# Kernel optimization log

Hardware: AMD Instinct MI355X
Metric: run time of the kernel (lower is better)

## Reference

```python
import jax, jax.numpy as jnp
import numpy as np

B, P, E, H = 32, 16, 50000, 128
EPS = 1e-5


def setup_inputs() -> dict:
    key = jax.random.key(0)
    ks = jax.random.split(key, 8)
    return {
        "inputs": jax.random.randint(ks[0], (B, P, E), 0, 2, dtype=jnp.int32),
        "emb": jax.random.normal(ks[1], (E, H), jnp.float32) * 0.02,
        "w1": jax.random.normal(ks[2], (H, H), jnp.float32) / np.sqrt(H),
        "b1": jax.random.normal(ks[3], (H,), jnp.float32) * 0.01,
        "w2": jax.random.normal(ks[4], (H, H), jnp.float32) / np.sqrt(H),
        "b2": jax.random.normal(ks[5], (H,), jnp.float32) * 0.01,
        "ln1_g": jnp.ones((H,), jnp.float32),
        "ln1_b": jnp.zeros((H,), jnp.float32),
        "ln2_g": jnp.ones((H,), jnp.float32),
        "ln2_b": jnp.zeros((H,), jnp.float32),
        "bn1_g": jnp.ones((H,), jnp.float32),
        "bn1_b": jnp.zeros((H,), jnp.float32),
        "bn2_g": jnp.ones((H,), jnp.float32),
        "bn2_b": jnp.zeros((H,), jnp.float32),
    }


def _layer_norm(x, g, b):
    mu = x.mean(-1, keepdims=True)
    var = ((x - mu) ** 2).mean(-1, keepdims=True)
    return g * (x - mu) / jnp.sqrt(var + EPS) + b


def _batch_norm_eval(x, g, b):
    # eval-mode BatchNorm1d with running_mean=0, running_var=1
    return g * x / jnp.sqrt(1.0 + EPS) + b


def reference(inputs, emb, w1, b1, w2, b2, ln1_g, ln1_b, ln2_g, ln2_b,
              bn1_g, bn1_b, bn2_g, bn2_b):
    # padding_idx=0: embedding row 0 is zero (but still counted in the mean,
    # matching the torch loop which averages over all selected indices)
    emb0 = emb.at[0].set(0.0)
    mask = (inputs == 1).astype(emb.dtype)            # [B, P, E] multi-hot
    sums = jnp.einsum("bpe,eh->bph", mask, emb0)       # segment-sum as one GEMM
    cnt = mask.sum(-1, keepdims=True)                  # [B, P, 1]
    path_emb = jnp.where(cnt > 0, sums / jnp.maximum(cnt, 1.0), 0.0)
    x = path_emb.mean(axis=1)                          # mean over paths -> [B, H]
    x = _layer_norm(x, ln1_g, ln1_b)
    x = jax.nn.relu(x @ w1.T + b1)
    x = _batch_norm_eval(x, bn1_g, bn1_b)              # dropout = identity (eval)
    x = _layer_norm(x, ln2_g, ln2_b)
    x = jax.nn.relu(x @ w2.T + b2)
    x = _batch_norm_eval(x, bn2_g, bn2_b)
    return x
```

## Files before the change

kernel.cpp:

```cpp
#include <hip/hip_runtime.h>
#include <stdint.h>

#define E_DIM 50000
#define EP    50048
#define HD    128
#define BD    32
#define PD    16
#define MD    512
#define BM    32
#define BK    64
#define KCHUNK 768
#define NKC   66
#define EPSF  1e-5f

typedef short short8 __attribute__((ext_vector_type(8)));
typedef float f32x4  __attribute__((ext_vector_type(4)));

__device__ __forceinline__ uint16_t f2bf(float f) {
  uint32_t u = __float_as_uint(f);
  u += 0x7FFFu + ((u >> 16) & 1u);
  return (uint16_t)(u >> 16);
}

__global__ __launch_bounds__(256) void k_embT(const float* __restrict__ emb,
                                              uint16_t* __restrict__ embT) {
  __shared__ __align__(16) uint16_t lds[HD * 64];
  const int t  = threadIdx.x;
  const int e0 = blockIdx.x * 64;

#pragma unroll
  for (int pass = 0; pass < 8; ++pass) {
    const int el = pass * 8 + (t >> 5);
    const int h  = (t & 31) * 4;
    const int eg = e0 + el;
    float4 v = {0.f, 0.f, 0.f, 0.f};
    if (eg < E_DIM && eg != 0)
      v = *(const float4*)(emb + (size_t)eg * HD + h);
    const uint16_t q0 = f2bf(v.x), q1 = f2bf(v.y), q2 = f2bf(v.z), q3 = f2bf(v.w);
    lds[(h + 0) * 64 + (el ^ (((h + 0) & 7) << 3))] = q0;
    lds[(h + 1) * 64 + (el ^ (((h + 1) & 7) << 3))] = q1;
    lds[(h + 2) * 64 + (el ^ (((h + 2) & 7) << 3))] = q2;
    lds[(h + 3) * 64 + (el ^ (((h + 3) & 7) << 3))] = q3;
  }
  __syncthreads();
#pragma unroll
  for (int pass = 0; pass < 8; ++pass) {
    const int hr  = pass * 16 + (t >> 4);
    const int el4 = (t & 15) * 4;
    uint2 d = *(const uint2*)(lds + hr * 64 + (el4 ^ ((hr & 7) << 3)));
    *(uint2*)(embT + (size_t)hr * EP + e0 + el4) = d;
  }
}

__global__ __launch_bounds__(256, 4) void k_gemm(const int* __restrict__ inp,
                                                 const uint16_t* __restrict__ embT,
                                                 float* __restrict__ part,
                                                 float* __restrict__ cntp) {
  __shared__ __align__(16) uint16_t ldsA[2][BM * BK];
  __shared__ __align__(16) uint16_t ldsB[2][HD * BK];

  const int t    = threadIdx.x;
  const int lane = t & 63;
  const int w    = t >> 6;

  const int virt = (blockIdx.x & 7) * (NKC * 16 / 8) + (blockIdx.x >> 3);
  const int mb = virt & 15;
  const int kc = virt >> 4;
  const int e0 = kc * KCHUNK;
  const int nst = min(12, (EP - e0) >> 6);

  const int sr = t >> 3;
  const int sc = (t & 7) * 8;
  const int* ap = inp + (size_t)(mb * BM + sr) * E_DIM + e0 + sc;
  const int aw = sr * 128 + (((t & 7) ^ (sr & 7)) << 4);

  const int bh = t >> 1;
  const int bq = (t & 1) * 4;
  const uint16_t* bp = embT + (size_t)bh * EP + e0 + bq * 8;
  const int bw0 = bh * 128 + (((bq + 0) ^ (bh & 7)) << 4);
  const int bw1 = bh * 128 + (((bq + 1) ^ (bh & 7)) << 4);
  const int bw2 = bh * 128 + (((bq + 2) ^ (bh & 7)) << 4);
  const int bw3 = bh * 128 + (((bq + 3) ^ (bh & 7)) << 4);

  const int r16 = lane & 15;
  const int kg  = (lane >> 4) << 3;
  const int aoff = r16 * 128;
  const int boff = (w * 32 + r16) * 128;
  const int swr  = r16 & 7;

  f32x4 acc00 = {0.f,0.f,0.f,0.f}, acc01 = {0.f,0.f,0.f,0.f};
  f32x4 acc10 = {0.f,0.f,0.f,0.f}, acc11 = {0.f,0.f,0.f,0.f};
  uint32_t cnt = 0;

  {
    int4 a0 = {0,0,0,0}, a1 = {0,0,0,0};
    if (e0 + sc < E_DIM) { a0 = *(const int4*)ap; a1 = *(const int4*)(ap + 4); }
    const short8 v0 = *(const short8*)(bp);
    const short8 v1 = *(const short8*)(bp + 8);
    const short8 v2 = *(const short8*)(bp + 16);
    const short8 v3 = *(const short8*)(bp + 24);
    const uint32_t w01 = (uint32_t)a0.x | ((uint32_t)a0.y << 16);
    const uint32_t w23 = (uint32_t)a0.z | ((uint32_t)a0.w << 16);
    const uint32_t w45 = (uint32_t)a1.x | ((uint32_t)a1.y << 16);
    const uint32_t w67 = (uint32_t)a1.z | ((uint32_t)a1.w << 16);
    cnt += w01 + w23 + w45 + w67;
    uint4 d = { w01 * 0x3F80u, w23 * 0x3F80u, w45 * 0x3F80u, w67 * 0x3F80u };
    *(uint4*)((char*)ldsA[0] + aw) = d;
    *(short8*)((char*)ldsB[0] + bw0) = v0;
    *(short8*)((char*)ldsB[0] + bw1) = v1;
    *(short8*)((char*)ldsB[0] + bw2) = v2;
    *(short8*)((char*)ldsB[0] + bw3) = v3;
    __syncthreads();
  }

  for (int s = 0; s < nst; ++s) {
    const int cur = s & 1;
    const int nxt = cur ^ 1;
    const bool hn = (s + 1 < nst);
    int4 a0 = {0,0,0,0}, a1 = {0,0,0,0};
    short8 v0, v1, v2, v3;
    if (hn) {
      const int off = (s + 1) * 64;
      if (e0 + off + sc < E_DIM) {
        a0 = *(const int4*)(ap + off);
        a1 = *(const int4*)(ap + off + 4);
      }
      v0 = *(const short8*)(bp + off);
      v1 = *(const short8*)(bp + off + 8);
      v2 = *(const short8*)(bp + off + 16);
      v3 = *(const short8*)(bp + off + 24);
    }

#pragma unroll
    for (int kk = 0; kk < 64; kk += 32) {
      const int cblk = (kk + kg) >> 3;
      const int sw16 = (cblk ^ swr) << 4;
      const short8 af0 = *(const short8*)((const char*)ldsA[cur] + aoff + sw16);
      const short8 af1 = *(const short8*)((const char*)ldsA[cur] + aoff + sw16 + 2048);
      const short8 bf0 = *(const short8*)((const char*)ldsB[cur] + boff + sw16);
      const short8 bf1 = *(const short8*)((const char*)ldsB[cur] + boff + sw16 + 2048);
      acc00 = __builtin_amdgcn_mfma_f32_16x16x32_bf16(af0, bf0, acc00, 0, 0, 0);
      acc01 = __builtin_amdgcn_mfma_f32_16x16x32_bf16(af0, bf1, acc01, 0, 0, 0);
      acc10 = __builtin_amdgcn_mfma_f32_16x16x32_bf16(af1, bf0, acc10, 0, 0, 0);
      acc11 = __builtin_amdgcn_mfma_f32_16x16x32_bf16(af1, bf1, acc11, 0, 0, 0);
    }

    if (hn) {
      const uint32_t w01 = (uint32_t)a0.x | ((uint32_t)a0.y << 16);
      const uint32_t w23 = (uint32_t)a0.z | ((uint32_t)a0.w << 16);
      const uint32_t w45 = (uint32_t)a1.x | ((uint32_t)a1.y << 16);
      const uint32_t w67 = (uint32_t)a1.z | ((uint32_t)a1.w << 16);
      cnt += w01 + w23 + w45 + w67;
      uint4 d = { w01 * 0x3F80u, w23 * 0x3F80u, w45 * 0x3F80u, w67 * 0x3F80u };
      *(uint4*)((char*)ldsA[nxt] + aw) = d;
      *(short8*)((char*)ldsB[nxt] + bw0) = v0;
      *(short8*)((char*)ldsB[nxt] + bw1) = v1;
      *(short8*)((char*)ldsB[nxt] + bw2) = v2;
      *(short8*)((char*)ldsB[nxt] + bw3) = v3;
    }
    __syncthreads();
  }

  {
    const int jr = (lane >> 4) << 2;
    float* pt0 = part + (size_t)kc * (MD * HD)
               + (size_t)(mb * BM + jr) * HD + w * 32 + r16;
#pragma unroll
    for (int j = 0; j < 4; ++j) {
      pt0[j * HD]             = acc00[j];
      pt0[j * HD + 16]        = acc01[j];
      pt0[(16 + j) * HD]      = acc10[j];
      pt0[(16 + j) * HD + 16] = acc11[j];
    }
  }

  {
    int c = (int)((cnt & 0xFFFFu) + (cnt >> 16));
    c += __shfl_xor(c, 1);
    c += __shfl_xor(c, 2);
    c += __shfl_xor(c, 4);
    if ((lane & 7) == 0)
      cntp[kc * MD + mb * BM + w * 8 + (lane >> 3)] = (float)c;
  }
}

__global__ __launch_bounds__(128) void k_reduce(const float* __restrict__ part,
                                                const float* __restrict__ cntp,
                                                float* __restrict__ pe) {
  const int r = blockIdx.x;
  const int t = threadIdx.x;
  const float* pp = part + (size_t)r * HD + t;
  float s = 0.f;
#pragma unroll 6
  for (int kc = 0; kc < NKC; ++kc) s += pp[(size_t)kc * (MD * HD)];
  float c = 0.f;
#pragma unroll 6
  for (int kc = 0; kc < NKC; ++kc) c += cntp[kc * MD + r];
  pe[r * HD + t] = (c > 0.f) ? (s / c) : 0.f;
}

__global__ __launch_bounds__(128) void k_tail(
    const float* __restrict__ pe,
    const float* __restrict__ w1, const float* __restrict__ b1,
    const float* __restrict__ w2, const float* __restrict__ b2,
    const float* __restrict__ ln1g, const float* __restrict__ ln1b,
    const float* __restrict__ ln2g, const float* __restrict__ ln2b,
    const float* __restrict__ bn1g, const float* __restrict__ bn1b,
    const float* __restrict__ bn2g, const float* __restrict__ bn2b,
    float* __restrict__ out) {
  const int b = blockIdx.x, t = threadIdx.x;
  __shared__ float sh[HD];
  __shared__ float red[HD];

  float x = 0.f;
#pragma unroll
  for (int p = 0; p < PD; ++p) x += pe[(b * PD + p) * HD + t];
  x *= (1.f / PD);

  const float bninv = rsqrtf(1.f + EPSF);

  red[t] = x; __syncthreads();
  for (int o = 64; o > 0; o >>= 1) { if (t < o) red[t] += red[t + o]; __syncthreads(); }
  const float mu1 = red[0] * (1.f / HD); __syncthreads();
  const float d1 = x - mu1;
  red[t] = d1 * d1; __syncthreads();
  for (int o = 64; o > 0; o >>= 1) { if (t < o) red[t] += red[t + o]; __syncthreads(); }
  const float v1 = red[0] * (1.f / HD); __syncthreads();
  const float y1 = ln1g[t] * d1 * rsqrtf(v1 + EPSF) + ln1b[t];

  sh[t] = y1; __syncthreads();
  float a = b1[t];
  const float4* wrow1 = (const float4*)(w1 + (size_t)t * HD);
#pragma unroll 8
  for (int k = 0; k < 32; ++k) {
    const float4 w = wrow1[k];
    a += w.x * sh[k * 4] + w.y * sh[k * 4 + 1] + w.z * sh[k * 4 + 2] + w.w * sh[k * 4 + 3];
  }
  a = fmaxf(a, 0.f);
  a = bn1g[t] * a * bninv + bn1b[t];
  __syncthreads();

  red[t] = a; __syncthreads();
  for (int o = 64; o > 0; o >>= 1) { if (t < o) red[t] += red[t + o]; __syncthreads(); }
  const float mu2 = red[0] * (1.f / HD); __syncthreads();
  const float d2 = a - mu2;
  red[t] = d2 * d2; __syncthreads();
  for (int o = 64; o > 0; o >>= 1) { if (t < o) red[t] += red[t + o]; __syncthreads(); }
  const float v2 = red[0] * (1.f / HD); __syncthreads();
  const float y2 = ln2g[t] * d2 * rsqrtf(v2 + EPSF) + ln2b[t];

  sh[t] = y2; __syncthreads();
  float a2 = b2[t];
  const float4* wrow2 = (const float4*)(w2 + (size_t)t * HD);
#pragma unroll 8
  for (int k = 0; k < 32; ++k) {
    const float4 w = wrow2[k];
    a2 += w.x * sh[k * 4] + w.y * sh[k * 4 + 1] + w.z * sh[k * 4 + 2] + w.w * sh[k * 4 + 3];
  }
  a2 = fmaxf(a2, 0.f);
  a2 = bn2g[t] * a2 * bninv + bn2b[t];
  out[b * HD + t] = a2;
}

extern "C" void kernel_launch(void* const* d_in, const int* in_sizes, int n_in,
                              void* d_out, int out_size, void* d_ws, size_t ws_size,
                              hipStream_t stream) {
  const int*   inp  = (const int*)d_in[0];
  const float* emb  = (const float*)d_in[1];
  const float* w1   = (const float*)d_in[2];
  const float* b1   = (const float*)d_in[3];
  const float* w2   = (const float*)d_in[4];
  const float* b2   = (const float*)d_in[5];
  const float* ln1g = (const float*)d_in[6];
  const float* ln1b = (const float*)d_in[7];
  const float* ln2g = (const float*)d_in[8];
  const float* ln2b = (const float*)d_in[9];
  const float* bn1g = (const float*)d_in[10];
  const float* bn1b = (const float*)d_in[11];
  const float* bn2g = (const float*)d_in[12];
  const float* bn2b = (const float*)d_in[13];
  float* out = (float*)d_out;

  char* ws = (char*)d_ws;
  uint16_t* embT = (uint16_t*)ws;
  float* part = (float*)(ws + 12812288);
  float* cntp = (float*)(ws + 12812288 + 17301504);
  float* pe   = (float*)(ws + 12812288 + 17301504 + 135168);

  k_embT<<<EP / 64, 256, 0, stream>>>(emb, embT);
  k_gemm<<<NKC * 16, 256, 0, stream>>>(inp, embT, part, cntp);
  k_reduce<<<MD, 128, 0, stream>>>(part, cntp, pe);
  k_tail<<<BD, 128, 0, stream>>>(pe, w1, b1, w2, b2, ln1g, ln1b, ln2g, ln2b,
                                 bn1g, bn1b, bn2g, bn2b, out);
}
```

Baseline: 67.77 us.

## Pre-pack embedding into MFMA fragment order and load B directly to registers

The embedding-conversion kernel now writes bf16 data in the exact per-lane MFMA fragment layout, so the GEMM loads B operands straight from global memory into registers. This removes the B tile's LDS staging and its shared-memory traffic. The main loop is also restructured into a two-stage register double buffer with explicit barriers and sched_barrier. The trade-off is higher register pressure under launch_bounds(256,4) and a slightly larger workspace, since the padded grid is 66*12 blocks.

```diff
diff --git a/kernel.cpp b/kernel.cpp
--- a/kernel.cpp
+++ b/kernel.cpp
@@ -11,6 +11,7 @@
 #define BK    64
 #define KCHUNK 768
 #define NKC   66
+#define NST   12
 #define EPSF  1e-5f
 
 typedef short short8 __attribute__((ext_vector_type(8)));
@@ -22,8 +23,8 @@
   return (uint16_t)(u >> 16);
 }
 
-__global__ __launch_bounds__(256) void k_embT(const float* __restrict__ emb,
-                                              uint16_t* __restrict__ embT) {
+__global__ __launch_bounds__(256) void k_embF(const float* __restrict__ emb,
+                                              uint16_t* __restrict__ embF) {
   __shared__ __align__(16) uint16_t lds[HD * 64];
   const int t  = threadIdx.x;
   const int e0 = blockIdx.x * 64;
@@ -43,21 +44,26 @@
     lds[(h + 3) * 64 + (el ^ (((h + 3) & 7) << 3))] = q3;
   }
   __syncthreads();
-#pragma unroll
-  for (int pass = 0; pass < 8; ++pass) {
-    const int hr  = pass * 16 + (t >> 4);
-    const int el4 = (t & 15) * 4;
-    uint2 d = *(const uint2*)(lds + hr * 64 + (el4 ^ ((hr & 7) << 3)));
-    *(uint2*)(embT + (size_t)hr * EP + e0 + el4) = d;
+
+  const int w    = t >> 6;
+  const int lane = t & 63;
+  const int r16  = lane & 15;
+  const int kgq  = (lane >> 4) * 8;
+  uint16_t* outp = embF + (size_t)blockIdx.x * 8192 + (size_t)w * 2048 + lane * 8;
+#pragma unroll
+  for (int fr = 0; fr < 4; ++fr) {
+    const int h  = (2 * w + (fr & 1)) * 16 + r16;
+    const int el = (fr >> 1) * 32 + kgq;
+    short8 d = *(const short8*)(lds + h * 64 + (el ^ ((h & 7) << 3)));
+    *(short8*)(outp + fr * 512) = d;
   }
 }
 
 __global__ __launch_bounds__(256, 4) void k_gemm(const int* __restrict__ inp,
-                                                 const uint16_t* __restrict__ embT,
+                                                 const uint16_t* __restrict__ embF,
                                                  float* __restrict__ part,
                                                  float* __restrict__ cntp) {
   __shared__ __align__(16) uint16_t ldsA[2][BM * BK];
-  __shared__ __align__(16) uint16_t ldsB[2][HD * BK];
 
   const int t    = threadIdx.x;
   const int lane = t & 63;
@@ -67,99 +73,92 @@
   const int mb = virt & 15;
   const int kc = virt >> 4;
   const int e0 = kc * KCHUNK;
-  const int nst = min(12, (EP - e0) >> 6);
+  const int nst = min(NST, (EP - e0) >> 6);
 
   const int sr = t >> 3;
   const int sc = (t & 7) * 8;
   const int* ap = inp + (size_t)(mb * BM + sr) * E_DIM + e0 + sc;
   const int aw = sr * 128 + (((t & 7) ^ (sr & 7)) << 4);
 
-  const int bh = t >> 1;
-  const int bq = (t & 1) * 4;
-  const uint16_t* bp = embT + (size_t)bh * EP + e0 + bq * 8;
-  const int bw0 = bh * 128 + (((bq + 0) ^ (bh & 7)) << 4);
-  const int bw1 = bh * 128 + (((bq + 1) ^ (bh & 7)) << 4);
-  const int bw2 = bh * 128 + (((bq + 2) ^ (bh & 7)) << 4);
-  const int bw3 = bh * 128 + (((bq + 3) ^ (bh & 7)) << 4);
-
-  const int r16 = lane & 15;
-  const int kg  = (lane >> 4) << 3;
+  const uint16_t* bp = embF + ((size_t)kc * NST) * 8192 + (size_t)w * 2048 + lane * 8;
+
+  const int r16  = lane & 15;
+  const int kg   = (lane >> 4) << 3;
   const int aoff = r16 * 128;
-  const int boff = (w * 32 + r16) * 128;
   const int swr  = r16 & 7;
 
   f32x4 acc00 = {0.f,0.f,0.f,0.f}, acc01 = {0.f,0.f,0.f,0.f};
   f32x4 acc10 = {0.f,0.f,0.f,0.f}, acc11 = {0.f,0.f,0.f,0.f};
   uint32_t cnt = 0;
 
-  {
-    int4 a0 = {0,0,0,0}, a1 = {0,0,0,0};
-    if (e0 + sc < E_DIM) { a0 = *(const int4*)ap; a1 = *(const int4*)(ap + 4); }
-    const short8 v0 = *(const short8*)(bp);
-    const short8 v1 = *(const short8*)(bp + 8);
-    const short8 v2 = *(const short8*)(bp + 16);
-    const short8 v3 = *(const short8*)(bp + 24);
-    const uint32_t w01 = (uint32_t)a0.x | ((uint32_t)a0.y << 16);
-    const uint32_t w23 = (uint32_t)a0.z | ((uint32_t)a0.w << 16);
-    const uint32_t w45 = (uint32_t)a1.x | ((uint32_t)a1.y << 16);
-    const uint32_t w67 = (uint32_t)a1.z | ((uint32_t)a1.w << 16);
-    cnt += w01 + w23 + w45 + w67;
-    uint4 d = { w01 * 0x3F80u, w23 * 0x3F80u, w45 * 0x3F80u, w67 * 0x3F80u };
-    *(uint4*)((char*)ldsA[0] + aw) = d;
-    *(short8*)((char*)ldsB[0] + bw0) = v0;
-    *(short8*)((char*)ldsB[0] + bw1) = v1;
-    *(short8*)((char*)ldsB[0] + bw2) = v2;
-    *(short8*)((char*)ldsB[0] + bw3) = v3;
-    __syncthreads();
-  }
-
-  for (int s = 0; s < nst; ++s) {
-    const int cur = s & 1;
-    const int nxt = cur ^ 1;
-    const bool hn = (s + 1 < nst);
-    int4 a0 = {0,0,0,0}, a1 = {0,0,0,0};
-    short8 v0, v1, v2, v3;
-    if (hn) {
-      const int off = (s + 1) * 64;
-      if (e0 + off + sc < E_DIM) {
-        a0 = *(const int4*)(ap + off);
-        a1 = *(const int4*)(ap + off + 4);
-      }
-      v0 = *(const short8*)(bp + off);
-      v1 = *(const short8*)(bp + off + 8);
-      v2 = *(const short8*)(bp + off + 16);
-      v3 = *(const short8*)(bp + off + 24);
-    }
-
-#pragma unroll
-    for (int kk = 0; kk < 64; kk += 32) {
-      const int cblk = (kk + kg) >> 3;
-      const int sw16 = (cblk ^ swr) << 4;
-      const short8 af0 = *(const short8*)((const char*)ldsA[cur] + aoff + sw16);
-      const short8 af1 = *(const short8*)((const char*)ldsA[cur] + aoff + sw16 + 2048);
-      const short8 bf0 = *(const short8*)((const char*)ldsB[cur] + boff + sw16);
-      const short8 bf1 = *(const short8*)((const char*)ldsB[cur] + boff + sw16 + 2048);
-      acc00 = __builtin_amdgcn_mfma_f32_16x16x32_bf16(af0, bf0, acc00, 0, 0, 0);
-      acc01 = __builtin_amdgcn_mfma_f32_16x16x32_bf16(af0, bf1, acc01, 0, 0, 0);
-      acc10 = __builtin_amdgcn_mfma_f32_16x16x32_bf16(af1, bf0, acc10, 0, 0, 0);
-      acc11 = __builtin_amdgcn_mfma_f32_16x16x32_bf16(af1, bf1, acc11, 0, 0, 0);
-    }
-
-    if (hn) {
-      const uint32_t w01 = (uint32_t)a0.x | ((uint32_t)a0.y << 16);
-      const uint32_t w23 = (uint32_t)a0.z | ((uint32_t)a0.w << 16);
-      const uint32_t w45 = (uint32_t)a1.x | ((uint32_t)a1.y << 16);
-      const uint32_t w67 = (uint32_t)a1.z | ((uint32_t)a1.w << 16);
-      cnt += w01 + w23 + w45 + w67;
-      uint4 d = { w01 * 0x3F80u, w23 * 0x3F80u, w45 * 0x3F80u, w67 * 0x3F80u };
-      *(uint4*)((char*)ldsA[nxt] + aw) = d;
-      *(short8*)((char*)ldsB[nxt] + bw0) = v0;
-      *(short8*)((char*)ldsB[nxt] + bw1) = v1;
-      *(short8*)((char*)ldsB[nxt] + bw2) = v2;
-      *(short8*)((char*)ldsB[nxt] + bw3) = v3;
-    }
-    __syncthreads();
-  }
+  int4 aP0x, aP0y, aP1x, aP1y;
+  short8 bP0[4], bP1[4];
+
+#define LOAD_A(DSTX, DSTY, SIG)                                   \
+  DSTX = (int4){0,0,0,0}; DSTY = (int4){0,0,0,0};                 \
+  if (e0 + (SIG) * 64 + sc < E_DIM) {                             \
+    DSTX = *(const int4*)(ap + (SIG) * 64);                       \
+    DSTY = *(const int4*)(ap + (SIG) * 64 + 4);                   \
+  }
+
+#define LOAD_B(DST, SIG)                                          \
+  _Pragma("unroll")                                               \
+  for (int fr = 0; fr < 4; ++fr)                                  \
+    DST[fr] = *(const short8*)(bp + (size_t)(SIG) * 8192 + fr * 512);
+
+#define CONVERT_WRITE_A(SRCX, SRCY, BUF, SIG)                     \
+  {                                                               \
+    const uint32_t w01 = (uint32_t)SRCX.x | ((uint32_t)SRCX.y << 16); \
+    const uint32_t w23 = (uint32_t)SRCX.z | ((uint32_t)SRCX.w << 16); \
+    const uint32_t w45 = (uint32_t)SRCY.x | ((uint32_t)SRCY.y << 16); \
+    const uint32_t w67 = (uint32_t)SRCY.z | ((uint32_t)SRCY.w << 16); \
+    cnt += w01 + w23 + w45 + w67;                                 \
+    uint4 d = { w01 * 0x3F80u, w23 * 0x3F80u, w45 * 0x3F80u, w67 * 0x3F80u }; \
+    *(uint4*)((char*)ldsA[BUF] + aw) = d;                         \
+  }
+
+#define BARRIER()                                                 \
+  asm volatile("s_waitcnt lgkmcnt(0)" ::: "memory");              \
+  __builtin_amdgcn_s_barrier();                                   \
+  __builtin_amdgcn_sched_barrier(0);
+
+#define MFMA_STAGE(BUF, BREG)                                     \
+  _Pragma("unroll")                                               \
+  for (int kk = 0; kk < 2; ++kk) {                                \
+    const int sw16 = (((kk * 4) + (kg >> 3)) ^ swr) << 4;         \
+    const short8 af0 = *(const short8*)((const char*)ldsA[BUF] + aoff + sw16); \
+    const short8 af1 = *(const short8*)((const char*)ldsA[BUF] + aoff + sw16 + 2048); \
+    acc00 = __builtin_amdgcn_mfma_f32_16x16x32_bf16(af0, BREG[kk*2+0], acc00, 0, 0, 0); \
+    acc01 = __builtin_amdgcn_mfma_f32_16x16x32_bf16(af0, BREG[kk*2+1], acc01, 0, 0, 0); \
+    acc10 = __builtin_amdgcn_mfma_f32_16x16x32_bf16(af1, BREG[kk*2+0], acc10, 0, 0, 0); \
+    acc11 = __builtin_amdgcn_mfma_f32_16x16x32_bf16(af1, BREG[kk*2+1], acc11, 0, 0, 0); \
+  }
+
+  LOAD_A(aP0x, aP0y, 0)
+  LOAD_A(aP1x, aP1y, 1)
+  LOAD_B(bP0, 0)
+  CONVERT_WRITE_A(aP0x, aP0y, 0, 0)
+  BARRIER()
+
+  for (int s = 0; s < nst; s += 2) {
+    if (s + 2 < nst) { LOAD_A(aP0x, aP0y, s + 2) }
+    if (s + 1 < nst) { LOAD_B(bP1, s + 1) }
+    MFMA_STAGE(0, bP0)
+    if (s + 1 < nst) { CONVERT_WRITE_A(aP1x, aP1y, 1, s + 1) }
+    BARRIER()
+
+    if (s + 3 < nst) { LOAD_A(aP1x, aP1y, s + 3) }
+    if (s + 2 < nst) { LOAD_B(bP0, s + 2) }
+    if (s + 1 < nst) { MFMA_STAGE(1, bP1) }
+    if (s + 2 < nst) { CONVERT_WRITE_A(aP0x, aP0y, 0, s + 2) }
+    BARRIER()
+  }
+
+#undef LOAD_A
+#undef LOAD_B
+#undef CONVERT_WRITE_A
+#undef BARRIER
+#undef MFMA_STAGE
 
   {
     const int jr = (lane >> 4) << 2;
@@ -282,13 +281,13 @@
   float* out = (float*)d_out;
 
   char* ws = (char*)d_ws;
-  uint16_t* embT = (uint16_t*)ws;
-  float* part = (float*)(ws + 12812288);
-  float* cntp = (float*)(ws + 12812288 + 17301504);
-  float* pe   = (float*)(ws + 12812288 + 17301504 + 135168);
-
-  k_embT<<<EP / 64, 256, 0, stream>>>(emb, embT);
-  k_gemm<<<NKC * 16, 256, 0, stream>>>(inp, embT, part, cntp);
+  uint16_t* embF = (uint16_t*)ws;
+  float* part = (float*)(ws + 12976128);
+  float* cntp = (float*)(ws + 12976128 + 17301504);
+  float* pe   = (float*)(ws + 12976128 + 17301504 + 135168);
+
+  k_embF<<<NKC * NST, 256, 0, stream>>>(emb, embF);
+  k_gemm<<<NKC * 16, 256, 0, stream>>>(inp, embF, part, cntp);
   k_reduce<<<MD, 128, 0, stream>>>(part, cntp, pe);
   k_tail<<<BD, 128, 0, stream>>>(pe, w1, b1, w2, b2, ln1g, ln1b, ln2g, ln2b,
                                  bn1g, bn1b, bn2g, bn2b, out);
```

New measurement: 59.64 us. 1.14x faster.
